# Kernel tuning notes

Measured on AMD Instinct MI355X. Metric: run time of the kernel, lower is better.

The kernel has to match this reference:

```python
import jax, jax.numpy as jnp
import numpy as np

N = 102400       # total nodes (1024 graphs x 100 nodes)
E = 1638400      # edges (avg degree 16)
B = 1024         # graphs; also GRU sequence length (unbatched 2D GRU input)
F_IN, HID, H1 = 4, 16, 6
OUT, FC1, RNN, ACT = 32, 64, 64, 11


def _gat(x, src, dst, W, a_src, a_dst, b, heads, out_dim, concat):
    # PyG GATConv (eval mode, dropout off), add_self_loops=True
    n = x.shape[0]
    loop = jnp.arange(n, dtype=src.dtype)
    s = jnp.concatenate([src, loop])
    d = jnp.concatenate([dst, loop])
    h = (x @ W.T).reshape(n, heads, out_dim)                 # [N,H,F]
    a_s = (h * a_src).sum(-1)                                # [N,H]
    a_d = (h * a_dst).sum(-1)                                # [N,H]
    e = jax.nn.leaky_relu(a_s[s] + a_d[d], 0.2)              # [E',H]
    m = jax.ops.segment_max(e, d, num_segments=n)
    p = jnp.exp(e - m[d])
    alpha = p / jax.ops.segment_sum(p, d, num_segments=n)[d]
    agg = jax.ops.segment_sum(h[s] * alpha[:, :, None], d, num_segments=n)  # [N,H,F]
    agg = agg.reshape(n, heads * out_dim) if concat else agg.mean(axis=1)
    return agg + b


def _gru(xs, wih, whh, bih, bhh):
    # torch nn.GRU, unbatched: xs is [L, FC1], h0 = zeros
    def step(hp, xt):
        gi = xt @ wih.T + bih
        gh = hp @ whh.T + bhh
        ir, iz, i_n = jnp.split(gi, 3)
        hr, hz, h_n = jnp.split(gh, 3)
        r = jax.nn.sigmoid(ir + hr)
        z = jax.nn.sigmoid(iz + hz)
        ng = jnp.tanh(i_n + r * h_n)
        h = (1.0 - z) * ng + z * hp
        return h, h
    _, ys = jax.lax.scan(step, jnp.zeros((RNN,), xs.dtype), xs)
    return ys


def setup_inputs():
    key = jax.random.key(0)
    ks = jax.random.split(key, 16)
    g = lambda i, shape, fan: jax.random.normal(ks[i], shape, jnp.float32) / np.sqrt(fan)
    x = jax.random.normal(ks[0], (N, F_IN), jnp.float32)
    src = jax.random.randint(ks[1], (E,), 0, N)
    dst = jax.random.randint(ks[2], (E,), 0, N)
    dst = jnp.where(dst == src, (dst + 1) % N, dst)  # no pre-existing self-loops
    edge_index = jnp.stack([src, dst]).astype(jnp.int32)
    robot_index = (jnp.arange(B) * (N // B)).astype(jnp.int32)  # ptr[:-1]
    robot_features = jax.random.normal(ks[3], (B, 4), jnp.float32)
    return dict(
        x=x, edge_index=edge_index, robot_index=robot_index, robot_features=robot_features,
        c1_W=g(4, (H1 * HID, F_IN), F_IN), c1_as=g(5, (H1, HID), HID), c1_ad=g(6, (H1, HID), HID),
        c1_b=jnp.zeros((H1 * HID,), jnp.float32),
        c2_W=g(7, (OUT, H1 * HID), H1 * HID), c2_as=g(8, (1, OUT), OUT), c2_ad=g(9, (1, OUT), OUT),
        c2_b=jnp.zeros((OUT,), jnp.float32),
        fc1_W=g(10, (FC1, OUT + 4), OUT + 4), fc1_b=jnp.zeros((FC1,), jnp.float32),
        gru_wih=g(11, (3 * RNN, FC1), FC1), gru_whh=g(12, (3 * RNN, RNN), RNN),
        gru_bih=jnp.zeros((3 * RNN,), jnp.float32), gru_bhh=jnp.zeros((3 * RNN,), jnp.float32),
        fc2_W=g(13, (ACT, RNN), RNN), fc2_b=jnp.zeros((ACT,), jnp.float32),
    )


def reference(x, edge_index, robot_index, robot_features,
              c1_W, c1_as, c1_ad, c1_b, c2_W, c2_as, c2_ad, c2_b,
              fc1_W, fc1_b, gru_wih, gru_whh, gru_bih, gru_bhh, fc2_W, fc2_b):
    src, dst = edge_index[0], edge_index[1]
    h = _gat(x, src, dst, c1_W, c1_as, c1_ad, c1_b, H1, HID, True)   # [N, 96]
    h = jnp.tanh(h)
    h = _gat(h, src, dst, c2_W, c2_as, c2_ad, c2_b, 1, OUT, False)   # [N, 32]
    h = h[robot_index]                                               # [B, 32]
    h = jnp.tanh(jnp.concatenate([h, robot_features], axis=1) @ fc1_W.T + fc1_b)  # [B, 64]
    h = _gru(h, gru_wih, gru_whh, gru_bih, gru_bhh)                  # [B, 64]
    return h @ fc2_W.T + fc2_b                                       # [B, 11] logits
```

## Files before the change

kernel.cpp:

```cpp
#include <hip/hip_runtime.h>

#define S2CAP 24576
#define DEG   96
#define CH    16

typedef float f32x4 __attribute__((ext_vector_type(4)));

__device__ __forceinline__ float fsig(float x){ return 1.f/(1.f + __expf(-x)); }
__device__ __forceinline__ float ftanh(float a){
  a = fminf(fmaxf(a, -15.f), 15.f);
  float e2 = __expf(2.f*a);
  return (e2 - 1.f)/(e2 + 1.f);
}
__device__ __forceinline__ float attw(float e){
  e = (e > 0.f) ? e : 0.2f*e;
  return __expf(e);
}

__global__ void k_init(const float* __restrict__ c1W, const float* __restrict__ c1as,
                       const float* __restrict__ c1ad, float* __restrict__ AsAd,
                       const int* __restrict__ rix, int B, int N, int* __restrict__ sidx,
                       int* __restrict__ nodeof, int* __restrict__ ctrl,
                       int* __restrict__ cnt1){
  int gid = blockIdx.x*blockDim.x + threadIdx.x;
  if (gid == 0) ctrl[0] = B;
  if (gid < 48){
    int which = gid/24, r = gid%24, k = r/6, h = r%6;
    const float* av = which ? c1ad : c1as;
    float s = 0.f;
    for (int f = 0; f < 16; ++f) s += c1W[(h*16+f)*4 + k] * av[h*16+f];
    AsAd[which*24 + k*6 + h] = s;
  }
  if (gid < S2CAP) cnt1[gid] = 0;
  for (int i = gid; i < N; i += gridDim.x*blockDim.x){
    int lo = 0, hi = B - 1, pos = -1;
    while (lo <= hi){
      int mid = (lo + hi) >> 1;
      int v = rix[mid];
      if (v == i){ pos = mid; break; }
      if (v < i) lo = mid + 1; else hi = mid - 1;
    }
    if (pos >= 0){ sidx[i] = pos; nodeof[pos] = i; }
    else sidx[i] = -1;
  }
}

__global__ void k_claim(const int* __restrict__ ei, int E, int B,
                        int* __restrict__ sidx, int* __restrict__ nodeof,
                        int* __restrict__ ctrl){
  int e = blockIdx.x*blockDim.x + threadIdx.x;
  if (e >= E) return;
  int d = ei[E + e];
  int sd = sidx[d];
  if (sd < 0 || sd >= B) return;
  int s = ei[e];
  if (sidx[s] < 0){
    int old = atomicCAS(&sidx[s], -1, -2);
    if (old == -1){
      int id = atomicAdd(&ctrl[0], 1);
      if (id < S2CAP){ nodeof[id] = s; sidx[s] = id; }
      else sidx[s] = -1;
    }
  }
}

__global__ void k_scat(const int* __restrict__ ei, int E,
                       const int* __restrict__ sidx, int* __restrict__ cnt1,
                       int* __restrict__ csr1){
  int e = blockIdx.x*blockDim.x + threadIdx.x;
  if (e >= E) return;
  int sd = sidx[ei[E + e]];
  if (sd >= 0){
    int p = atomicAdd(&cnt1[sd], 1);
    if (p < DEG) csr1[sd*DEG + p] = ei[e];
  }
}

__global__ __launch_bounds__(256) void k_gath2(const float* __restrict__ x,
                       const float* __restrict__ c1W, const float* __restrict__ c1b,
                       const float* __restrict__ AsAd, const int* __restrict__ nodeof,
                       const int* __restrict__ cnt1, const int* __restrict__ csr1,
                       const int* __restrict__ ctrl, const float* __restrict__ c2W,
                       const float* __restrict__ c2as, const float* __restrict__ c2ad,
                       float* __restrict__ h2, float* __restrict__ as2,
                       float* __restrict__ ad2){
  __shared__ float tl[8][96];
  int tid = threadIdx.x;
  int base = blockIdx.x*8;
  int nsid = ctrl[0];
  if (tid < 48){
    int sl = tid/6, h = tid - sl*6;
    int sid = base + sl;
    if (sid < nsid){
      float Ask[4], Adk[4];
      #pragma unroll
      for (int k = 0; k < 4; ++k){ Ask[k] = AsAd[k*6+h]; Adk[k] = AsAd[24 + k*6 + h]; }
      float W[16][4];
      #pragma unroll
      for (int f = 0; f < 16; ++f)
        #pragma unroll
        for (int k = 0; k < 4; ++k) W[f][k] = c1W[(h*16+f)*4 + k];
      int d = nodeof[sid];
      float4 xd = *(const float4*)(x + 4*(size_t)d);
      float ad = xd.x*Adk[0] + xd.y*Adk[1] + xd.z*Adk[2] + xd.w*Adk[3];
      int beg = sid*DEG, n = cnt1[sid];
      n = (n < DEG) ? n : DEG;
      float den = 0.f, agg[16];
      #pragma unroll
      for (int f = 0; f < 16; ++f) agg[f] = 0.f;
      for (int j = -1; j < n; ++j){
        int s = (j < 0) ? d : csr1[beg + j];
        float4 xv = *(const float4*)(x + 4*(size_t)s);
        float as = xv.x*Ask[0] + xv.y*Ask[1] + xv.z*Ask[2] + xv.w*Ask[3];
        float wgt = attw(as + ad);
        den += wgt;
        #pragma unroll
        for (int f = 0; f < 16; ++f){
          float h1 = xv.x*W[f][0] + xv.y*W[f][1] + xv.z*W[f][2] + xv.w*W[f][3];
          agg[f] = fmaf(wgt, h1, agg[f]);
        }
      }
      float inv = 1.f/den;
      #pragma unroll
      for (int f = 0; f < 16; ++f)
        tl[sl][h*16 + f] = ftanh(agg[f]*inv + c1b[h*16+f]);
    }
  }
  __syncthreads();
  int sl = tid >> 5, o = tid & 31;
  int sid = base + sl;
  bool act = sid < nsid;
  float s = 0.f;
  if (act){
    const float* t = tl[sl];
    const float* wr = c2W + o*96;
    #pragma unroll
    for (int j = 0; j < 96; ++j) s = fmaf(wr[j], t[j], s);
    h2[(size_t)sid*32 + o] = s;
  }
  float a = act ? s*c2as[o] : 0.f;
  float b = act ? s*c2ad[o] : 0.f;
  #pragma unroll
  for (int w = 16; w >= 1; w >>= 1){
    a += __shfl_xor(a, w, 32);
    b += __shfl_xor(b, w, 32);
  }
  if (act && o == 0){ as2[sid] = a; ad2[sid] = b; }
}

__global__ __launch_bounds__(192) void k_g2g(const float* __restrict__ h2,
                        const float* __restrict__ as2, const float* __restrict__ ad2,
                        const float* __restrict__ c2b, const float* __restrict__ rf,
                        const float* __restrict__ fc1W, const float* __restrict__ fc1b,
                        const int* __restrict__ sidx, const int* __restrict__ cnt1,
                        const int* __restrict__ csr1, const float* __restrict__ wih,
                        const float* __restrict__ bih, const float* __restrict__ bhh,
                        float* __restrict__ gi){
  int rp = blockIdx.x, tid = threadIdx.x;
  __shared__ float cat[36];
  __shared__ float xsl[64];
  float ad = ad2[rp];
  int beg = rp*DEG, n = cnt1[rp];
  n = (n < DEG) ? n : DEG;
  if (tid < 32){
    int o = tid;
    float den = 0.f, agg = 0.f;
    for (int j = -1; j < n; ++j){
      int ss;
      if (j < 0) ss = rp;
      else { int s = csr1[beg + j]; ss = sidx[s]; if (ss < 0 || ss >= S2CAP) continue; }
      float wgt = attw(as2[ss] + ad);
      den += wgt;
      agg = fmaf(wgt, h2[(size_t)ss*32 + o], agg);
    }
    cat[o] = agg/den + c2b[o];
    if (o < 4) cat[32 + o] = rf[rp*4 + o];
  }
  __syncthreads();
  if (tid < 64){
    float s = fc1b[tid];
    const float* wrow = fc1W + tid*36;
    #pragma unroll
    for (int j = 0; j < 36; ++j) s = fmaf(wrow[j], cat[j], s);
    xsl[tid] = ftanh(s);
  }
  __syncthreads();
  {
    int g = tid;
    const float* wr = wih + (size_t)g*64;
    float s = bih[g] + (g < 128 ? bhh[g] : 0.f);
    #pragma unroll
    for (int k = 0; k < 64; ++k) s = fmaf(wr[k], xsl[k], s);
    gi[(size_t)rp*192 + g] = s;
  }
}

__global__ __launch_bounds__(192, 1) void k_gru3(const float* __restrict__ gi,
                       const float* __restrict__ whh, const float* __restrict__ bhh,
                       float* __restrict__ ys, const float* __restrict__ f2W,
                       const float* __restrict__ f2b, float* __restrict__ out, int B){
  int tid = threadIdx.x;
  int w = tid >> 6, u = tid & 63, g = tid;
  const float* p = whh + (size_t)g*64;
  f32x4 w0,w1,w2,w3,w4,w5,w6,w7,w8,w9,w10,w11,w12,w13,w14,w15;
#define LDW(R, OFF) asm volatile("global_load_dwordx4 %0, %1, off offset:" #OFF : "=v"(R) : "v"(p))
  LDW(w0,0);    LDW(w1,16);   LDW(w2,32);   LDW(w3,48);
  LDW(w4,64);   LDW(w5,80);   LDW(w6,96);   LDW(w7,112);
  LDW(w8,128);  LDW(w9,144);  LDW(w10,160); LDW(w11,176);
  LDW(w12,192); LDW(w13,208); LDW(w14,224); LDW(w15,240);
#undef LDW
  asm volatile("s_waitcnt vmcnt(0)" ::: "memory");
  __builtin_amdgcn_sched_barrier(0);
  float bb = (w == 2) ? bhh[128 + u] : 0.f;

  __shared__ float gbuf[3][CH*192];
  __shared__ float rzbuf[2][256];
  int nch = (B + CH - 1)/CH;

  auto stage = [&](int cbuf, int chunk){
    if (chunk >= nch) return;
    const float* gb = gi + (size_t)chunk*(CH*192) + w*1024 + u*4;
    float* lb = &gbuf[cbuf][w*1024];
    __builtin_amdgcn_global_load_lds(
      (const __attribute__((address_space(1))) unsigned int*)(gb),
      (__attribute__((address_space(3))) unsigned int*)(lb), 16, 0, 0);
    __builtin_amdgcn_global_load_lds(
      (const __attribute__((address_space(1))) unsigned int*)(gb + 256),
      (__attribute__((address_space(3))) unsigned int*)(lb + 256), 16, 0, 0);
    __builtin_amdgcn_global_load_lds(
      (const __attribute__((address_space(1))) unsigned int*)(gb + 512),
      (__attribute__((address_space(3))) unsigned int*)(lb + 512), 16, 0, 0);
    __builtin_amdgcn_global_load_lds(
      (const __attribute__((address_space(1))) unsigned int*)(gb + 768),
      (__attribute__((address_space(3))) unsigned int*)(lb + 768), 16, 0, 0);
  };

  stage(0, 0);
  stage(1, 1);

  float hvec = 0.f, gcur = 0.f;
#define PIN(R) asm volatile("" : "+v"(R))
#define DOT4(W, K)                                                    \
  { float h0_ = __int_as_float(__builtin_amdgcn_readlane(hb, (K)));   \
    float h1_ = __int_as_float(__builtin_amdgcn_readlane(hb, (K)+1)); \
    float h2_ = __int_as_float(__builtin_amdgcn_readlane(hb, (K)+2)); \
    float h3_ = __int_as_float(__builtin_amdgcn_readlane(hb, (K)+3)); \
    a0 = fmaf(W.x, h0_, a0); a1 = fmaf(W.y, h1_, a1);                 \
    a2 = fmaf(W.z, h2_, a2); a3 = fmaf(W.w, h3_, a3); }

  int cbx = 0;
  for (int c = 0; c < nch; ++c){
    int nbx = cbx + 1; if (nbx == 3) nbx = 0;
    int sbx = nbx + 1; if (sbx == 3) sbx = 0;
    asm volatile("s_waitcnt vmcnt(0)" ::: "memory");
    __syncthreads();
    stage(sbx, c + 2);
    if (c == 0) gcur = gbuf[0][g];
    int lim = B - c*CH; if (lim > CH) lim = CH;
    for (int ti = 0; ti < lim; ++ti){
      int t = c*CH + ti;
      PIN(w0); PIN(w1); PIN(w2);  PIN(w3);  PIN(w4);  PIN(w5);  PIN(w6);  PIN(w7);
      PIN(w8); PIN(w9); PIN(w10); PIN(w11); PIN(w12); PIN(w13); PIN(w14); PIN(w15);
      float gnext = (ti + 1 < CH) ? gbuf[cbx][(ti+1)*192 + g] : gbuf[nbx][g];
      float a0 = 0.f, a1 = 0.f, a2 = 0.f, a3 = 0.f;
      int hb = __float_as_int(hvec);
      DOT4(w0,0);   DOT4(w1,4);   DOT4(w2,8);   DOT4(w3,12);
      DOT4(w4,16);  DOT4(w5,20);  DOT4(w6,24);  DOT4(w7,28);
      DOT4(w8,32);  DOT4(w9,36);  DOT4(w10,40); DOT4(w11,44);
      DOT4(w12,48); DOT4(w13,52); DOT4(w14,56); DOT4(w15,60);
      float dot = (a0 + a1) + (a2 + a3);
      float* buf = rzbuf[t & 1];
      if (w < 2){
        buf[w*64 + u] = gcur + dot;
      } else {
        buf[128 + u] = dot + bb;
        buf[192 + u] = gcur;
      }
      __syncthreads();
      float pre_r = buf[u], pre_z = buf[64 + u], an = buf[128 + u], i_n = buf[192 + u];
      float r  = fsig(pre_r);
      float z  = fsig(pre_z);
      float ng = ftanh(i_n + r*an);
      float hnew = (1.f - z)*ng + z*hvec;
      if (w == 2) ys[(size_t)t*64 + u] = hnew;
      hvec = hnew;
      gcur = gnext;
    }
    cbx = nbx;
  }
#undef PIN
#undef DOT4
  asm volatile("s_waitcnt vmcnt(0)" ::: "memory");
  __syncthreads();
  for (int idx = tid; idx < B*11; idx += 192){
    int t = idx/11, a = idx - t*11;
    const float* hv = ys + (size_t)t*64;
    const float* wr = f2W + a*64;
    float s = f2b[a];
    #pragma unroll
    for (int k = 0; k < 64; ++k) s = fmaf(wr[k], hv[k], s);
    out[idx] = s;
  }
}

extern "C" void kernel_launch(void* const* d_in, const int* in_sizes, int n_in,
                              void* d_out, int out_size, void* d_ws, size_t ws_size,
                              hipStream_t stream) {
  (void)n_in; (void)out_size; (void)ws_size;
  const float* x    = (const float*)d_in[0];
  const int*   ei   = (const int*)d_in[1];
  const int*   rix  = (const int*)d_in[2];
  const float* rf   = (const float*)d_in[3];
  const float* c1W  = (const float*)d_in[4];
  const float* c1as = (const float*)d_in[5];
  const float* c1ad = (const float*)d_in[6];
  const float* c1b  = (const float*)d_in[7];
  const float* c2W  = (const float*)d_in[8];
  const float* c2as = (const float*)d_in[9];
  const float* c2ad = (const float*)d_in[10];
  const float* c2b  = (const float*)d_in[11];
  const float* fc1W = (const float*)d_in[12];
  const float* fc1b = (const float*)d_in[13];
  const float* wih  = (const float*)d_in[14];
  const float* whh  = (const float*)d_in[15];
  const float* bih  = (const float*)d_in[16];
  const float* bhh  = (const float*)d_in[17];
  const float* f2W  = (const float*)d_in[18];
  const float* f2b  = (const float*)d_in[19];
  float* out = (float*)d_out;

  const int N = in_sizes[0]/4;
  const int E = in_sizes[1]/2;
  const int B = in_sizes[2];

  char* w = (char*)d_ws;
  size_t off = 0;
  auto take = [&](size_t bytes)->char*{
    char* p = w + off;
    off = (off + bytes + 255) & ~(size_t)255;
    return p;
  };
  int*   ctrl   = (int*)  take(256);
  float* AsAd   = (float*)take(256);
  int*   sidx   = (int*)  take((size_t)N*4);
  int*   nodeof = (int*)  take((size_t)S2CAP*4);
  int*   cnt1   = (int*)  take((size_t)S2CAP*4);
  int*   csr1   = (int*)  take((size_t)S2CAP*DEG*4);
  float* h2     = (float*)take((size_t)S2CAP*32*4);
  float* as2    = (float*)take((size_t)S2CAP*4);
  float* ad2    = (float*)take((size_t)S2CAP*4);
  float* gi     = (float*)take((size_t)B*192*4);
  float* ys     = (float*)take((size_t)B*64*4);

  k_init  <<<(N+255)/256, 256, 0, stream>>>(c1W, c1as, c1ad, AsAd, rix, B, N, sidx, nodeof, ctrl, cnt1);
  k_claim <<<(E+255)/256, 256, 0, stream>>>(ei, E, B, sidx, nodeof, ctrl);
  k_scat  <<<(E+255)/256, 256, 0, stream>>>(ei, E, sidx, cnt1, csr1);
  k_gath2 <<<S2CAP/8, 256, 0, stream>>>(x, c1W, c1b, AsAd, nodeof, cnt1, csr1, ctrl, c2W, c2as, c2ad, h2, as2, ad2);
  k_g2g   <<<B, 192, 0, stream>>>(h2, as2, ad2, c2b, rf, fc1W, fc1b, sidx, cnt1, csr1, wih, bih, bhh, gi);
  k_gru3  <<<1, 192, 0, stream>>>(gi, whh, bhh, ys, f2W, f2b, out, B);
}
```

Before: 985.4 us.

## Run GRU recurrence in a single wavefront and split fc2 into its own kernel

New measurement: 1.196 ms. 21.3% more time.

```diff
diff --git a/kernel.cpp b/kernel.cpp
--- a/kernel.cpp
+++ b/kernel.cpp
@@ -2,7 +2,6 @@
 
 #define S2CAP 24576
 #define DEG   96
-#define CH    16
 
 typedef float f32x4 __attribute__((ext_vector_type(4)));
 
@@ -195,112 +194,88 @@
   }
 }
 
-__global__ __launch_bounds__(192, 1) void k_gru3(const float* __restrict__ gi,
-                       const float* __restrict__ whh, const float* __restrict__ bhh,
-                       float* __restrict__ ys, const float* __restrict__ f2W,
-                       const float* __restrict__ f2b, float* __restrict__ out, int B){
-  int tid = threadIdx.x;
-  int w = tid >> 6, u = tid & 63, g = tid;
-  const float* p = whh + (size_t)g*64;
-  f32x4 w0,w1,w2,w3,w4,w5,w6,w7,w8,w9,w10,w11,w12,w13,w14,w15;
-#define LDW(R, OFF) asm volatile("global_load_dwordx4 %0, %1, off offset:" #OFF : "=v"(R) : "v"(p))
-  LDW(w0,0);    LDW(w1,16);   LDW(w2,32);   LDW(w3,48);
-  LDW(w4,64);   LDW(w5,80);   LDW(w6,96);   LDW(w7,112);
-  LDW(w8,128);  LDW(w9,144);  LDW(w10,160); LDW(w11,176);
-  LDW(w12,192); LDW(w13,208); LDW(w14,224); LDW(w15,240);
+__global__ __launch_bounds__(64)
+__attribute__((amdgpu_waves_per_eu(1, 1), amdgpu_flat_work_group_size(64, 64)))
+void k_gru1(const float* __restrict__ gi, const float* __restrict__ whh,
+            const float* __restrict__ bhh, float* __restrict__ ys, int B){
+  int u = threadIdx.x;
+  const float* pr = whh + (size_t)u*64;
+  const float* pz = whh + (size_t)(64 + u)*64;
+  const float* pn = whh + (size_t)(128 + u)*64;
+  f32x4 r0,r1,r2,r3,r4,r5,r6,r7,r8,r9,r10,r11,r12,r13,r14,r15;
+  f32x4 z0,z1,z2,z3,z4,z5,z6,z7,z8,z9,z10,z11,z12,z13,z14,z15;
+  f32x4 n0,n1,n2,n3,n4,n5,n6,n7,n8,n9,n10,n11,n12,n13,n14,n15;
+#define LDW(R, P, OFF) asm volatile("global_load_dwordx4 %0, %1, off offset:" #OFF : "=v"(R) : "v"(P))
+  LDW(r0,pr,0);    LDW(r1,pr,16);   LDW(r2,pr,32);   LDW(r3,pr,48);
+  LDW(r4,pr,64);   LDW(r5,pr,80);   LDW(r6,pr,96);   LDW(r7,pr,112);
+  LDW(r8,pr,128);  LDW(r9,pr,144);  LDW(r10,pr,160); LDW(r11,pr,176);
+  LDW(r12,pr,192); LDW(r13,pr,208); LDW(r14,pr,224); LDW(r15,pr,240);
+  LDW(z0,pz,0);    LDW(z1,pz,16);   LDW(z2,pz,32);   LDW(z3,pz,48);
+  LDW(z4,pz,64);   LDW(z5,pz,80);   LDW(z6,pz,96);   LDW(z7,pz,112);
+  LDW(z8,pz,128);  LDW(z9,pz,144);  LDW(z10,pz,160); LDW(z11,pz,176);
+  LDW(z12,pz,192); LDW(z13,pz,208); LDW(z14,pz,224); LDW(z15,pz,240);
+  LDW(n0,pn,0);    LDW(n1,pn,16);   LDW(n2,pn,32);   LDW(n3,pn,48);
+  LDW(n4,pn,64);   LDW(n5,pn,80);   LDW(n6,pn,96);   LDW(n7,pn,112);
+  LDW(n8,pn,128);  LDW(n9,pn,144);  LDW(n10,pn,160); LDW(n11,pn,176);
+  LDW(n12,pn,192); LDW(n13,pn,208); LDW(n14,pn,224); LDW(n15,pn,240);
 #undef LDW
   asm volatile("s_waitcnt vmcnt(0)" ::: "memory");
   __builtin_amdgcn_sched_barrier(0);
-  float bb = (w == 2) ? bhh[128 + u] : 0.f;
-
-  __shared__ float gbuf[3][CH*192];
-  __shared__ float rzbuf[2][256];
-  int nch = (B + CH - 1)/CH;
-
-  auto stage = [&](int cbuf, int chunk){
-    if (chunk >= nch) return;
-    const float* gb = gi + (size_t)chunk*(CH*192) + w*1024 + u*4;
-    float* lb = &gbuf[cbuf][w*1024];
-    __builtin_amdgcn_global_load_lds(
-      (const __attribute__((address_space(1))) unsigned int*)(gb),
-      (__attribute__((address_space(3))) unsigned int*)(lb), 16, 0, 0);
-    __builtin_amdgcn_global_load_lds(
-      (const __attribute__((address_space(1))) unsigned int*)(gb + 256),
-      (__attribute__((address_space(3))) unsigned int*)(lb + 256), 16, 0, 0);
-    __builtin_amdgcn_global_load_lds(
-      (const __attribute__((address_space(1))) unsigned int*)(gb + 512),
-      (__attribute__((address_space(3))) unsigned int*)(lb + 512), 16, 0, 0);
-    __builtin_amdgcn_global_load_lds(
-      (const __attribute__((address_space(1))) unsigned int*)(gb + 768),
-      (__attribute__((address_space(3))) unsigned int*)(lb + 768), 16, 0, 0);
-  };
-
-  stage(0, 0);
-  stage(1, 1);
-
-  float hvec = 0.f, gcur = 0.f;
+  float bn = bhh[128 + u];
+  float hu = 0.f;
+  float gr = gi[u], gz = gi[64 + u], gn = gi[128 + u];
 #define PIN(R) asm volatile("" : "+v"(R))
-#define DOT4(W, K)                                                    \
+#define DOT12(RW, ZW, NW, K)                                          \
   { float h0_ = __int_as_float(__builtin_amdgcn_readlane(hb, (K)));   \
     float h1_ = __int_as_float(__builtin_amdgcn_readlane(hb, (K)+1)); \
     float h2_ = __int_as_float(__builtin_amdgcn_readlane(hb, (K)+2)); \
     float h3_ = __int_as_float(__builtin_amdgcn_readlane(hb, (K)+3)); \
-    a0 = fmaf(W.x, h0_, a0); a1 = fmaf(W.y, h1_, a1);                 \
-    a2 = fmaf(W.z, h2_, a2); a3 = fmaf(W.w, h3_, a3); }
-
-  int cbx = 0;
-  for (int c = 0; c < nch; ++c){
-    int nbx = cbx + 1; if (nbx == 3) nbx = 0;
-    int sbx = nbx + 1; if (sbx == 3) sbx = 0;
-    asm volatile("s_waitcnt vmcnt(0)" ::: "memory");
-    __syncthreads();
-    stage(sbx, c + 2);
-    if (c == 0) gcur = gbuf[0][g];
-    int lim = B - c*CH; if (lim > CH) lim = CH;
-    for (int ti = 0; ti < lim; ++ti){
-      int t = c*CH + ti;
-      PIN(w0); PIN(w1); PIN(w2);  PIN(w3);  PIN(w4);  PIN(w5);  PIN(w6);  PIN(w7);
-      PIN(w8); PIN(w9); PIN(w10); PIN(w11); PIN(w12); PIN(w13); PIN(w14); PIN(w15);
-      float gnext = (ti + 1 < CH) ? gbuf[cbx][(ti+1)*192 + g] : gbuf[nbx][g];
-      float a0 = 0.f, a1 = 0.f, a2 = 0.f, a3 = 0.f;
-      int hb = __float_as_int(hvec);
-      DOT4(w0,0);   DOT4(w1,4);   DOT4(w2,8);   DOT4(w3,12);
-      DOT4(w4,16);  DOT4(w5,20);  DOT4(w6,24);  DOT4(w7,28);
-      DOT4(w8,32);  DOT4(w9,36);  DOT4(w10,40); DOT4(w11,44);
-      DOT4(w12,48); DOT4(w13,52); DOT4(w14,56); DOT4(w15,60);
-      float dot = (a0 + a1) + (a2 + a3);
-      float* buf = rzbuf[t & 1];
-      if (w < 2){
-        buf[w*64 + u] = gcur + dot;
-      } else {
-        buf[128 + u] = dot + bb;
-        buf[192 + u] = gcur;
-      }
-      __syncthreads();
-      float pre_r = buf[u], pre_z = buf[64 + u], an = buf[128 + u], i_n = buf[192 + u];
-      float r  = fsig(pre_r);
-      float z  = fsig(pre_z);
-      float ng = ftanh(i_n + r*an);
-      float hnew = (1.f - z)*ng + z*hvec;
-      if (w == 2) ys[(size_t)t*64 + u] = hnew;
-      hvec = hnew;
-      gcur = gnext;
-    }
-    cbx = nbx;
+    ar0 = fmaf(RW.x, h0_, ar0); az0 = fmaf(ZW.x, h0_, az0); an0 = fmaf(NW.x, h0_, an0); \
+    ar1 = fmaf(RW.y, h1_, ar1); az1 = fmaf(ZW.y, h1_, az1); an1 = fmaf(NW.y, h1_, an1); \
+    ar2 = fmaf(RW.z, h2_, ar2); az2 = fmaf(ZW.z, h2_, az2); an2 = fmaf(NW.z, h2_, an2); \
+    ar3 = fmaf(RW.w, h3_, ar3); az3 = fmaf(ZW.w, h3_, az3); an3 = fmaf(NW.w, h3_, an3); }
+  for (int t = 0; t < B; ++t){
+    PIN(r0); PIN(r1); PIN(r2);  PIN(r3);  PIN(r4);  PIN(r5);  PIN(r6);  PIN(r7);
+    PIN(r8); PIN(r9); PIN(r10); PIN(r11); PIN(r12); PIN(r13); PIN(r14); PIN(r15);
+    PIN(z0); PIN(z1); PIN(z2);  PIN(z3);  PIN(z4);  PIN(z5);  PIN(z6);  PIN(z7);
+    PIN(z8); PIN(z9); PIN(z10); PIN(z11); PIN(z12); PIN(z13); PIN(z14); PIN(z15);
+    PIN(n0); PIN(n1); PIN(n2);  PIN(n3);  PIN(n4);  PIN(n5);  PIN(n6);  PIN(n7);
+    PIN(n8); PIN(n9); PIN(n10); PIN(n11); PIN(n12); PIN(n13); PIN(n14); PIN(n15);
+    int tn = (t + 1 < B) ? t + 1 : t;
+    float grn = gi[tn*192 + u], gzn = gi[tn*192 + 64 + u], gnn = gi[tn*192 + 128 + u];
+    float ar0 = gr, ar1 = 0.f, ar2 = 0.f, ar3 = 0.f;
+    float az0 = gz, az1 = 0.f, az2 = 0.f, az3 = 0.f;
+    float an0 = bn, an1 = 0.f, an2 = 0.f, an3 = 0.f;
+    int hb = __float_as_int(hu);
+    DOT12(r0, z0, n0, 0);   DOT12(r1, z1, n1, 4);   DOT12(r2, z2, n2, 8);
+    DOT12(r3, z3, n3, 12);  DOT12(r4, z4, n4, 16);  DOT12(r5, z5, n5, 20);
+    DOT12(r6, z6, n6, 24);  DOT12(r7, z7, n7, 28);  DOT12(r8, z8, n8, 32);
+    DOT12(r9, z9, n9, 36);  DOT12(r10,z10,n10,40);  DOT12(r11,z11,n11,44);
+    DOT12(r12,z12,n12,48);  DOT12(r13,z13,n13,52);  DOT12(r14,z14,n14,56);
+    DOT12(r15,z15,n15,60);
+    float r  = fsig((ar0 + ar1) + (ar2 + ar3));
+    float z  = fsig((az0 + az1) + (az2 + az3));
+    float an = (an0 + an1) + (an2 + an3);
+    float ng = ftanh(gn + r*an);
+    hu = ng + z*(hu - ng);
+    ys[(size_t)t*64 + u] = hu;
+    gr = grn; gz = gzn; gn = gnn;
   }
 #undef PIN
-#undef DOT4
-  asm volatile("s_waitcnt vmcnt(0)" ::: "memory");
-  __syncthreads();
-  for (int idx = tid; idx < B*11; idx += 192){
-    int t = idx/11, a = idx - t*11;
-    const float* hv = ys + (size_t)t*64;
-    const float* wr = f2W + a*64;
-    float s = f2b[a];
-    #pragma unroll
-    for (int k = 0; k < 64; ++k) s = fmaf(wr[k], hv[k], s);
-    out[idx] = s;
-  }
+#undef DOT12
+}
+
+__global__ void k_fc2(const float* __restrict__ ys, const float* __restrict__ f2W,
+                      const float* __restrict__ f2b, float* __restrict__ out, int B){
+  int gid = blockIdx.x*blockDim.x + threadIdx.x;
+  if (gid >= B*11) return;
+  int t = gid/11, a = gid - t*11;
+  const float* hv = ys + (size_t)t*64;
+  const float* wr = f2W + a*64;
+  float s = f2b[a];
+  #pragma unroll
+  for (int k = 0; k < 64; ++k) s = fmaf(wr[k], hv[k], s);
+  out[gid] = s;
 }
 
 extern "C" void kernel_launch(void* const* d_in, const int* in_sizes, int n_in,
@@ -357,5 +332,6 @@
   k_scat  <<<(E+255)/256, 256, 0, stream>>>(ei, E, sidx, cnt1, csr1);
   k_gath2 <<<S2CAP/8, 256, 0, stream>>>(x, c1W, c1b, AsAd, nodeof, cnt1, csr1, ctrl, c2W, c2as, c2ad, h2, as2, ad2);
   k_g2g   <<<B, 192, 0, stream>>>(h2, as2, ad2, c2b, rf, fc1W, fc1b, sidx, cnt1, csr1, wih, bih, bhh, gi);
-  k_gru3  <<<1, 192, 0, stream>>>(gi, whh, bhh, ys, f2W, f2b, out, B);
-}
+  k_gru1  <<<1, 64, 0, stream>>>(gi, whh, bhh, ys, B);
+  k_fc2   <<<(B*11+255)/256, 256, 0, stream>>>(ys, f2W, f2b, out, B);
+}
```
